# Optimization experiments

Measured on AMD Instinct MI355X. Metric: run time of the kernel, lower is better.

## Reference

```python
import jax, jax.numpy as jnp
import numpy as np

HEADS = 16
DIM_HEAD = 64
SCALE = DIM_HEAD ** -0.5


def setup_inputs() -> dict:
    key = jax.random.key(0)
    k1, k2, k3 = jax.random.split(key, 3)
    B, N, D = 8, 1024, 1024
    x = jax.random.normal(k1, (B, N, D), dtype=jnp.float32)
    # 0/1 keep-mask over the N-1 non-prepended positions
    mask = jax.random.randint(k2, (B, N - 1), 0, 2, dtype=jnp.int32)
    # Linear(dim, 3*inner_dim, bias=False); stored as [dim, 3*inner] so y = x @ W
    w_qkv = jax.random.normal(k3, (D, 3 * HEADS * DIM_HEAD), dtype=jnp.float32) * (D ** -0.5)
    return {"x": x, "mask": mask, "w_qkv": w_qkv}


def reference(x, mask, w_qkv):
    b, n, _ = x.shape
    h, d = HEADS, DIM_HEAD
    qkv = x @ w_qkv                                    # [b, n, 3*h*d]
    q, k, v = jnp.split(qkv, 3, axis=-1)
    to_heads = lambda t: t.reshape(b, n, h, d).transpose(0, 2, 1, 3)  # b h n d
    q, k, v = to_heads(q), to_heads(k), to_heads(v)
    dots = jnp.einsum('bhid,bhjd->bhij', q, k) * SCALE  # [b, h, n, n]
    # F.pad(mask.flatten(1), (1,0), value=1.0) -> prepend a kept position
    m = jnp.pad(mask.reshape(b, -1).astype(jnp.float32), ((0, 0), (1, 0)),
                constant_values=1.0)                    # [b, n]
    dots = dots - 10000.0 * (1.0 - m)[:, None, None, :]
    attn = jax.nn.softmax(dots, axis=-1)
    out = jnp.einsum('bhij,bhjd->bhid', attn, v)        # [b, h, n, d]
    return out.transpose(0, 2, 1, 3).reshape(b, n, h * d)
```

## Files before the change

### kernel.cpp

```cpp
#include <hip/hip_runtime.h>
#include <hip/hip_bf16.h>
#include <stdint.h>

#define HEADS 16
#define DH    64
#define SEQ   1024
#define DIM   1024

typedef __attribute__((ext_vector_type(8))) short bf16x8;
typedef __attribute__((ext_vector_type(4))) float f32x4;
typedef __attribute__((ext_vector_type(16))) float f32x16;
typedef __attribute__((ext_vector_type(4))) unsigned int u32x4;

#define QSCALE_L2 0.18033688011112042f
#define THR_L2 11.541560327111707f
#define PEN_L2 (-14427.0f)

static __device__ __forceinline__ unsigned short f2bf(float f) {
  unsigned u = __builtin_bit_cast(unsigned, f);
  u += 0x7fff + ((u >> 16) & 1);
  return (unsigned short)(u >> 16);
}

static __device__ __forceinline__ float fexp2(float x) {
#if __has_builtin(__builtin_amdgcn_exp2f)
  return __builtin_amdgcn_exp2f(x);
#else
  return exp2f(x);
#endif
}

static __device__ __forceinline__ void gload_lds16(const void* g, void* l) {
  __builtin_amdgcn_global_load_lds(
      (const __attribute__((address_space(1))) unsigned int*)g,
      (__attribute__((address_space(3))) unsigned int*)l,
      16, 0, 0);
}

__global__ __launch_bounds__(256) void build_keep(
    const int* __restrict__ mask, int* __restrict__ inv,
    unsigned short* __restrict__ penc, int* __restrict__ nkeep) {
  const int b = blockIdx.x;
  const int t = threadIdx.x;
  __shared__ int sc[256];
  int kept[4];
  int c = 0;
#pragma unroll
  for (int k = 0; k < 4; ++k) {
    const int j = t * 4 + k;
    const int kp = (j == 0) ? 1 : (mask[b * (SEQ - 1) + j - 1] != 0);
    kept[k] = kp;
    c += kp;
  }
  sc[t] = c;
  __syncthreads();
  for (int off = 1; off < 256; off <<= 1) {
    const int v = (t >= off) ? sc[t - off] : 0;
    __syncthreads();
    sc[t] += v;
    __syncthreads();
  }
  int pos = sc[t] - c;
  const int total = sc[255];
#pragma unroll
  for (int k = 0; k < 4; ++k) {
    const int j = t * 4 + k;
    if (kept[k]) {
      inv[b * SEQ + j] = pos++;
    } else {
      inv[b * SEQ + j] = -1;
    }
  }
#pragma unroll
  for (int k = 0; k < 4; ++k) {
    const int i = t * 4 + k;
    penc[b * SEQ + i] = (i < total) ? (unsigned short)0 : f2bf(PEN_L2);
  }
  if (t == 0) nkeep[b] = total;
}

__global__ __launch_bounds__(256) void cvt_x(
    const float* __restrict__ in, unsigned short* __restrict__ out) {
  const int i = (blockIdx.x * 256 + threadIdx.x) * 4;
  const float4 v = *reinterpret_cast<const float4*>(in + i);
  short4 o;
  o.x = (short)f2bf(v.x);
  o.y = (short)f2bf(v.y);
  o.z = (short)f2bf(v.z);
  o.w = (short)f2bf(v.w);
  *reinterpret_cast<short4*>(out + i) = o;
}

__global__ __launch_bounds__(256) void transpose_w(
    const float* __restrict__ w, unsigned short* __restrict__ wT) {
  __shared__ unsigned short t[64][68];
  const int tid = threadIdx.x;
  const int bk = blockIdx.x;
  const int bn = blockIdx.y;
  const int r = tid >> 4;
  const int c = (tid & 15) * 4;
#pragma unroll
  for (int rr = 0; rr < 64; rr += 16) {
    const float4 v = *reinterpret_cast<const float4*>(
        w + (size_t)(bk * 64 + r + rr) * 3072 + bn * 64 + c);
    t[r + rr][c + 0] = f2bf(v.x);
    t[r + rr][c + 1] = f2bf(v.y);
    t[r + rr][c + 2] = f2bf(v.z);
    t[r + rr][c + 3] = f2bf(v.w);
  }
  __syncthreads();
#pragma unroll
  for (int rr = 0; rr < 64; rr += 16) {
    short4 o;
    o.x = (short)t[c + 0][r + rr];
    o.y = (short)t[c + 1][r + rr];
    o.z = (short)t[c + 2][r + rr];
    o.w = (short)t[c + 3][r + rr];
    *reinterpret_cast<short4*>(
        wT + (size_t)(bn * 64 + r + rr) * 1024 + bk * 64 + c) = o;
  }
}

__global__ __launch_bounds__(256) void qkv_gemm(
    const unsigned short* __restrict__ x, const unsigned short* __restrict__ wT,
    const int* __restrict__ inv,
    unsigned short* __restrict__ Qh, unsigned short* __restrict__ Kc,
    unsigned short* __restrict__ Vtc) {
  __shared__ unsigned short Al[128 * 32];
  __shared__ unsigned short Bl[128 * 32];
  const int tid = threadIdx.x;
  const int lane = tid & 63;
  const int wave = tid >> 6;
  const int m0 = blockIdx.x * 128;
  const int n0 = blockIdx.y * 128;
  const int wm = (wave >> 1) * 64;
  const int wn = (wave & 1) * 64;
  const int l15 = lane & 15;
  const int kb8 = (lane >> 4) * 8;

  f32x4 acc[4][4] = {};

  for (int kt = 0; kt < DIM; kt += 32) {
    __syncthreads();
#pragma unroll
    for (int rnd = 0; rnd < 2; ++rnd) {
      const int off = tid * 16 + rnd * 4096;
      const int row = off >> 6;
      const int kc = (off & 63) >> 1;
      gload_lds16(x + (size_t)(m0 + row) * DIM + kt + kc, (char*)Al + off);
      gload_lds16(wT + (size_t)(n0 + row) * DIM + kt + kc, (char*)Bl + off);
    }
    __syncthreads();
    bf16x8 af[4], bfr[4];
#pragma unroll
    for (int i = 0; i < 4; ++i)
      af[i] = *reinterpret_cast<const bf16x8*>(&Al[(wm + i * 16 + l15) * 32 + kb8]);
#pragma unroll
    for (int j = 0; j < 4; ++j)
      bfr[j] = *reinterpret_cast<const bf16x8*>(&Bl[(wn + j * 16 + l15) * 32 + kb8]);
#pragma unroll
    for (int i = 0; i < 4; ++i)
#pragma unroll
      for (int j = 0; j < 4; ++j)
        acc[i][j] = __builtin_amdgcn_mfma_f32_16x16x32_bf16(af[i], bfr[j], acc[i][j], 0, 0, 0);
  }

  const int sec = n0 >> 10;
  if (sec == 0) {
#pragma unroll
    for (int i = 0; i < 4; ++i) {
#pragma unroll
      for (int j = 0; j < 4; ++j) {
        const int col = n0 + wn + j * 16 + l15;
        const int h = (col >> 6) & 15;
        const int dh = col & 63;
#pragma unroll
        for (int r = 0; r < 4; ++r) {
          const int rowg = m0 + wm + i * 16 + (lane >> 4) * 4 + r;
          const int b = rowg >> 10;
          const int n = rowg & 1023;
          Qh[(((size_t)b * HEADS + h) * SEQ + n) * DH + dh] =
              f2bf(acc[i][j][r] * QSCALE_L2);
        }
      }
    }
  } else {
    int ivr[4][4];
#pragma unroll
    for (int i = 0; i < 4; ++i)
#pragma unroll
      for (int r = 0; r < 4; ++r) {
        const int rowg = m0 + wm + i * 16 + (lane >> 4) * 4 + r;
        ivr[i][r] = inv[(rowg >> 10) * SEQ + (rowg & 1023)];
      }
    if (sec == 1) {
#pragma unroll
      for (int i = 0; i < 4; ++i) {
#pragma unroll
        for (int j = 0; j < 4; ++j) {
          const int col = n0 + wn + j * 16 + l15;
          const int h = (col >> 6) & 15;
          const int dh = col & 63;
#pragma unroll
          for (int r = 0; r < 4; ++r) {
            const int rowg = m0 + wm + i * 16 + (lane >> 4) * 4 + r;
            const int b = rowg >> 10;
            const int iv = ivr[i][r];
            if (iv >= 0)
              Kc[(((size_t)b * HEADS + h) * SEQ + iv) * DH + dh] =
                  f2bf(acc[i][j][r]);
          }
        }
      }
    } else {
#pragma unroll
      for (int i = 0; i < 4; ++i) {
#pragma unroll
        for (int j = 0; j < 4; ++j) {
          const int col = n0 + wn + j * 16 + l15;
          const int h = (col >> 6) & 15;
          const int dh = col & 63;
#pragma unroll
          for (int r = 0; r < 4; ++r) {
            const int rowg = m0 + wm + i * 16 + (lane >> 4) * 4 + r;
            const int b = rowg >> 10;
            const int iv = ivr[i][r];
            if (iv >= 0)
              Vtc[(((size_t)b * HEADS + h) * DH + dh) * SEQ + iv] =
                  f2bf(acc[i][j][r]);
          }
        }
      }
    }
  }
}

__global__ __launch_bounds__(256) void attn_fwd4(
    const unsigned short* __restrict__ Qh, const unsigned short* __restrict__ Kc,
    const unsigned short* __restrict__ Vtc, const unsigned short* __restrict__ penc,
    const int* __restrict__ nkeep, float* __restrict__ out) {
  __shared__ alignas(16) unsigned char Kl[2][8192];
  __shared__ alignas(16) unsigned char Vl[2][8192];
  __shared__ unsigned short penb[SEQ];
  __shared__ float corrw[4][32];
  const int tid = threadIdx.x;
  const int lane = tid & 63;
  const int wave = tid >> 6;
  const int l31 = lane & 31;
  const int hi = lane >> 5;
  const int h8 = hi * 8;
  const bool islo = lane < 32;

  const int bid = ((blockIdx.x & 7) << 7) | (blockIdx.x >> 3);
  const int b = bid >> 7;
  const int hh = (bid >> 3) & 15;
  const int qc = bid & 7;
  const size_t bh = (size_t)b * HEADS + hh;
  const int q0 = qc * 128 + wave * 32;

  const int nk = nkeep[b];
  const int ntile = (nk + 63) >> 6;

  const unsigned short* Q = Qh + bh * SEQ * DH;
  const unsigned short* K = Kc + bh * SEQ * DH;
  const unsigned short* V = Vtc + bh * DH * SEQ;

  auto STAGE = [&](int buf, int kt) {
#pragma unroll
    for (int p = 0; p < 2; ++p) {
      const int off = p * 4096 + tid * 16;
      const int row = off >> 7;
      const int chunk = (off >> 4) & 7;
      const int sch = chunk ^ (row & 7);
      gload_lds16(K + (size_t)(kt + row) * DH + sch * 8, &Kl[buf][off]);
      gload_lds16(V + (size_t)row * SEQ + kt + sch * 8, &Vl[buf][off]);
    }
  };

  STAGE(0, 0);
  for (int j = tid; j < SEQ; j += 256) penb[j] = penc[b * SEQ + j];

  bf16x8 qf[4];
#pragma unroll
  for (int ds = 0; ds < 4; ++ds)
    qf[ds] = *reinterpret_cast<const bf16x8*>(
        Q + (size_t)(q0 + l31) * DH + ds * 16 + h8);

  u32x4 onesu = {0u, 0u, 0u, 0u};
  onesu.x = islo ? 0x3F80u : 0u;
  const bf16x8 onesf = __builtin_bit_cast(bf16x8, onesu);

  f32x16 Od0 = (f32x16)0.f, Od1 = (f32x16)0.f;
  float m_ = 0.f, l_ = 0.f;

  __syncthreads();

  int cur = 0;
  for (int ti = 0; ti < ntile; ++ti) {
    const int kt = ti * 64;
    if (ti + 1 < ntile) STAGE(cur ^ 1, kt + 64);

    f32x16 st0 = (f32x16)0.f, st1 = (f32x16)0.f;
    __builtin_amdgcn_s_setprio(1);
#pragma unroll
    for (int ds = 0; ds < 4; ++ds) {
      const int c0 = (ds * 2 + hi) ^ (l31 & 7);
      const bf16x8 kf0 = *reinterpret_cast<const bf16x8*>(
          &Kl[cur][l31 * 128 + c0 * 16]);
      st0 = __builtin_amdgcn_mfma_f32_32x32x16_bf16(kf0, qf[ds], st0, 0, 0, 0);
      const bf16x8 kf1 = *reinterpret_cast<const bf16x8*>(
          &Kl[cur][(32 + l31) * 128 + c0 * 16]);
      st1 = __builtin_amdgcn_mfma_f32_32x32x16_bf16(kf1, qf[ds], st1, 0, 0, 0);
    }
    __builtin_amdgcn_s_setprio(0);

    {
      const unsigned short pu0 = penb[kt + l31];
      const unsigned short pu1 = penb[kt + 32 + l31];
      u32x4 p0 = {0u, 0u, 0u, 0u}, p1 = {0u, 0u, 0u, 0u};
      p0.x = islo ? (unsigned)pu0 : 0u;
      p1.x = islo ? (unsigned)pu1 : 0u;
      st0 = __builtin_amdgcn_mfma_f32_32x32x16_bf16(
          __builtin_bit_cast(bf16x8, p0), onesf, st0, 0, 0, 0);
      st1 = __builtin_amdgcn_mfma_f32_32x32x16_bf16(
          __builtin_bit_cast(bf16x8, p1), onesf, st1, 0, 0, 0);
    }
    float a[8];
#pragma unroll
    for (int i = 0; i < 8; ++i)
      a[i] = fmaxf(fmaxf(st0[i], st0[i + 8]), fmaxf(st1[i], st1[i + 8]));
#pragma unroll
    for (int k = 4; k >= 1; k >>= 1)
#pragma unroll
      for (int i = 0; i < k; ++i) a[i] = fmaxf(a[i], a[i + k]);
    const float mx = fmaxf(a[0], __shfl_xor(a[0], 32));
    if (!__all(mx <= m_ + THR_L2)) {
      const float mn = fmaxf(m_, mx);
      const float corr = fexp2(m_ - mn);
      m_ = mn;
      l_ *= corr;
      if (islo) corrw[wave][l31] = corr;
      f32x4 cv[4];
#pragma unroll
      for (int j = 0; j < 4; ++j)
        cv[j] = *reinterpret_cast<const f32x4*>(&corrw[wave][j * 8 + (h8 >> 1)]);
#pragma unroll
      for (int r = 0; r < 16; ++r) {
        Od0[r] *= cv[r >> 2][r & 3];
        Od1[r] *= cv[r >> 2][r & 3];
      }
    }
#pragma unroll
    for (int i = 0; i < 16; ++i) {
      st0[i] = fexp2(st0[i] - m_);
      st1[i] = fexp2(st1[i] - m_);
    }
    float s8[8];
#pragma unroll
    for (int i = 0; i < 8; ++i)
      s8[i] = (st0[i] + st0[i + 8]) + (st1[i] + st1[i + 8]);
#pragma unroll
    for (int k = 4; k >= 1; k >>= 1)
#pragma unroll
      for (int i = 0; i < k; ++i) s8[i] += s8[i + k];
    l_ += s8[0] + __shfl_xor(s8[0], 32);
    bf16x8 pf[4];
#pragma unroll
    for (int t = 0; t < 2; ++t) {
#pragma unroll
      for (int bq = 0; bq < 2; ++bq) {
        const int o = 8 * bq;
        float e0 = t ? st1[o + 0] : st0[o + 0], e1 = t ? st1[o + 1] : st0[o + 1];
        float e2 = t ? st1[o + 2] : st0[o + 2], e3 = t ? st1[o + 3] : st0[o + 3];
        float e4 = t ? st1[o + 4] : st0[o + 4], e5 = t ? st1[o + 5] : st0[o + 5];
        float e6 = t ? st1[o + 6] : st0[o + 6], e7 = t ? st1[o + 7] : st0[o + 7];
        unsigned A0, A1, B0, B1;
        asm("v_cvt_pk_bf16_f32 %0, %1, %2" : "=v"(A0) : "v"(e0), "v"(e1));
        asm("v_cvt_pk_bf16_f32 %0, %1, %2" : "=v"(A1) : "v"(e2), "v"(e3));
        asm("v_cvt_pk_bf16_f32 %0, %1, %2" : "=v"(B0) : "v"(e4), "v"(e5));
        asm("v_cvt_pk_bf16_f32 %0, %1, %2" : "=v"(B1) : "v"(e6), "v"(e7));
        asm("v_permlane32_swap_b32 %0, %1\n\ts_nop 1" : "+v"(A0), "+v"(B0));
        asm("v_permlane32_swap_b32 %0, %1\n\ts_nop 1" : "+v"(A1), "+v"(B1));
        u32x4 pk4;
        pk4.x = A0; pk4.y = A1; pk4.z = B0; pk4.w = B1;
        pf[t * 2 + bq] = __builtin_bit_cast(bf16x8, pk4);
      }
    }
    __builtin_amdgcn_s_setprio(1);
#pragma unroll
    for (int kvs = 0; kvs < 4; ++kvs) {
      const int c0 = (kvs * 2 + hi) ^ (l31 & 7);
      const bf16x8 v0 = *reinterpret_cast<const bf16x8*>(
          &Vl[cur][l31 * 128 + c0 * 16]);
      Od0 = __builtin_amdgcn_mfma_f32_32x32x16_bf16(pf[kvs], v0, Od0, 0, 0, 0);
      const bf16x8 v1 = *reinterpret_cast<const bf16x8*>(
          &Vl[cur][(32 + l31) * 128 + c0 * 16]);
      Od1 = __builtin_amdgcn_mfma_f32_32x32x16_bf16(pf[kvs], v1, Od1, 0, 0, 0);
    }
    __builtin_amdgcn_s_setprio(0);

    __syncthreads();
    cur ^= 1;
  }

  if (islo) corrw[wave][l31] = 1.0f / l_;
  f32x4 lv[4];
#pragma unroll
  for (int j = 0; j < 4; ++j)
    lv[j] = *reinterpret_cast<const f32x4*>(&corrw[wave][j * 8 + (h8 >> 1)]);
#pragma unroll
  for (int r = 0; r < 16; ++r) {
    const int q = q0 + (r & 3) + 8 * (r >> 2) + (hi << 2);
    out[((size_t)b * SEQ + q) * (HEADS * DH) + hh * DH + 0 * 32 + l31] =
        Od0[r] * lv[r >> 2][r & 3];
    out[((size_t)b * SEQ + q) * (HEADS * DH) + hh * DH + 1 * 32 + l31] =
        Od1[r] * lv[r >> 2][r & 3];
  }
}

extern "C" void kernel_launch(void* const* d_in, const int* in_sizes, int n_in,
                              void* d_out, int out_size, void* d_ws, size_t ws_size,
                              hipStream_t stream) {
  const float* x = (const float*)d_in[0];
  const int* mask = (const int*)d_in[1];
  const float* w = (const float*)d_in[2];
  float* outp = (float*)d_out;

  char* ws = (char*)d_ws;
  unsigned short* xb   = (unsigned short*)(ws);
  unsigned short* wT   = (unsigned short*)(ws + 16777216);
  unsigned short* Qh   = (unsigned short*)(ws + 23068672);
  unsigned short* Kc   = (unsigned short*)(ws + 39845888);
  unsigned short* Vtc  = (unsigned short*)(ws + 56623104);
  int*            inv  = (int*)(ws + 73400320);
  unsigned short* penc = (unsigned short*)(ws + 73433088);
  int*            nkp  = (int*)(ws + 73449472);

  build_keep<<<dim3(8), 256, 0, stream>>>(mask, inv, penc, nkp);
  cvt_x<<<dim3(8192), 256, 0, stream>>>(x, xb);
  transpose_w<<<dim3(16, 48), 256, 0, stream>>>(w, wT);
  qkv_gemm<<<dim3(64, 24), 256, 0, stream>>>(xb, wT, inv, Qh, Kc, Vtc);
  attn_fwd4<<<dim3(1024), 256, 0, stream>>>(Qh, Kc, Vtc, penc, nkp, outp);
}
```

Baseline: 140.7 us.

## Stage GEMM epilogue through LDS for vector stores, add separate V transpose kernel

The QKV GEMM epilogue now writes each 16x64 accumulator block into shared memory and reads it back as 16-byte rows, so Q, K and V are stored with vectorised, coalesced writes instead of scattered 2-byte stores. The strided transposed V write is replaced by a row-major compacted V buffer plus a new transpose_v kernel that builds the transposed layout in the reused x workspace. The per-key penalty array is removed and the mask penalty is computed inline, applied only on the last key tile. This adds an extra kernel launch and an extra pass over V in exchange for removing uncoalesced global stores.

Result: faster. 131.7 us (-6.4%).

```diff
diff --git a/kernel.cpp b/kernel.cpp
--- a/kernel.cpp
+++ b/kernel.cpp
@@ -38,8 +38,7 @@
 }
 
 __global__ __launch_bounds__(256) void build_keep(
-    const int* __restrict__ mask, int* __restrict__ inv,
-    unsigned short* __restrict__ penc, int* __restrict__ nkeep) {
+    const int* __restrict__ mask, int* __restrict__ inv, int* __restrict__ nkeep) {
   const int b = blockIdx.x;
   const int t = threadIdx.x;
   __shared__ int sc[256];
@@ -65,16 +64,8 @@
 #pragma unroll
   for (int k = 0; k < 4; ++k) {
     const int j = t * 4 + k;
-    if (kept[k]) {
-      inv[b * SEQ + j] = pos++;
-    } else {
-      inv[b * SEQ + j] = -1;
-    }
-  }
-#pragma unroll
-  for (int k = 0; k < 4; ++k) {
-    const int i = t * 4 + k;
-    penc[b * SEQ + i] = (i < total) ? (unsigned short)0 : f2bf(PEN_L2);
+    inv[b * SEQ + j] = kept[k] ? pos : -1;
+    pos += kept[k];
   }
   if (t == 0) nkeep[b] = total;
 }
@@ -125,7 +116,7 @@
     const unsigned short* __restrict__ x, const unsigned short* __restrict__ wT,
     const int* __restrict__ inv,
     unsigned short* __restrict__ Qh, unsigned short* __restrict__ Kc,
-    unsigned short* __restrict__ Vtc) {
+    unsigned short* __restrict__ Vc) {
   __shared__ unsigned short Al[128 * 32];
   __shared__ unsigned short Bl[128 * 32];
   const int tid = threadIdx.x;
@@ -137,6 +128,7 @@
   const int wn = (wave & 1) * 64;
   const int l15 = lane & 15;
   const int kb8 = (lane >> 4) * 8;
+  const int lg4 = (lane >> 4) * 4;
 
   f32x4 acc[4][4] = {};
 
@@ -165,83 +157,75 @@
         acc[i][j] = __builtin_amdgcn_mfma_f32_16x16x32_bf16(af[i], bfr[j], acc[i][j], 0, 0, 0);
   }
 
+  __syncthreads();
+  unsigned short* Sw = (wave < 2 ? Al : Bl) + (wave & 1) * (16 * 72);
   const int sec = n0 >> 10;
-  if (sec == 0) {
-#pragma unroll
-    for (int i = 0; i < 4; ++i) {
-#pragma unroll
-      for (int j = 0; j < 4; ++j) {
-        const int col = n0 + wn + j * 16 + l15;
-        const int h = (col >> 6) & 15;
-        const int dh = col & 63;
-#pragma unroll
-        for (int r = 0; r < 4; ++r) {
-          const int rowg = m0 + wm + i * 16 + (lane >> 4) * 4 + r;
-          const int b = rowg >> 10;
-          const int n = rowg & 1023;
-          Qh[(((size_t)b * HEADS + h) * SEQ + n) * DH + dh] =
-              f2bf(acc[i][j][r] * QSCALE_L2);
+  const float sc = (sec == 0) ? QSCALE_L2 : 1.0f;
+  const int h = ((n0 + wn) >> 6) & 15;
+#pragma unroll
+  for (int i = 0; i < 4; ++i) {
+#pragma unroll
+    for (int j = 0; j < 4; ++j)
+#pragma unroll
+      for (int r = 0; r < 4; ++r)
+        Sw[(lg4 + r) * 72 + j * 16 + l15] = f2bf(acc[i][j][r] * sc);
+#pragma unroll
+    for (int pass = 0; pass < 2; ++pass) {
+      const int row = pass * 8 + (lane >> 3);
+      const int chunk = lane & 7;
+      const bf16x8 vv = *reinterpret_cast<const bf16x8*>(&Sw[row * 72 + chunk * 8]);
+      const int grow = m0 + wm + i * 16 + row;
+      const int b = grow >> 10;
+      const int n = grow & 1023;
+      const size_t bh = (size_t)b * HEADS + h;
+      if (sec == 0) {
+        *reinterpret_cast<bf16x8*>(&Qh[(bh * SEQ + n) * DH + chunk * 8]) = vv;
+      } else {
+        const int iv = inv[b * SEQ + n];
+        if (iv >= 0) {
+          if (sec == 1)
+            *reinterpret_cast<bf16x8*>(&Kc[(bh * SEQ + iv) * DH + chunk * 8]) = vv;
+          else
+            *reinterpret_cast<bf16x8*>(&Vc[(bh * SEQ + iv) * DH + chunk * 8]) = vv;
         }
       }
     }
-  } else {
-    int ivr[4][4];
-#pragma unroll
-    for (int i = 0; i < 4; ++i)
-#pragma unroll
-      for (int r = 0; r < 4; ++r) {
-        const int rowg = m0 + wm + i * 16 + (lane >> 4) * 4 + r;
-        ivr[i][r] = inv[(rowg >> 10) * SEQ + (rowg & 1023)];
-      }
-    if (sec == 1) {
-#pragma unroll
-      for (int i = 0; i < 4; ++i) {
-#pragma unroll
-        for (int j = 0; j < 4; ++j) {
-          const int col = n0 + wn + j * 16 + l15;
-          const int h = (col >> 6) & 15;
-          const int dh = col & 63;
-#pragma unroll
-          for (int r = 0; r < 4; ++r) {
-            const int rowg = m0 + wm + i * 16 + (lane >> 4) * 4 + r;
-            const int b = rowg >> 10;
-            const int iv = ivr[i][r];
-            if (iv >= 0)
-              Kc[(((size_t)b * HEADS + h) * SEQ + iv) * DH + dh] =
-                  f2bf(acc[i][j][r]);
-          }
-        }
-      }
-    } else {
-#pragma unroll
-      for (int i = 0; i < 4; ++i) {
-#pragma unroll
-        for (int j = 0; j < 4; ++j) {
-          const int col = n0 + wn + j * 16 + l15;
-          const int h = (col >> 6) & 15;
-          const int dh = col & 63;
-#pragma unroll
-          for (int r = 0; r < 4; ++r) {
-            const int rowg = m0 + wm + i * 16 + (lane >> 4) * 4 + r;
-            const int b = rowg >> 10;
-            const int iv = ivr[i][r];
-            if (iv >= 0)
-              Vtc[(((size_t)b * HEADS + h) * DH + dh) * SEQ + iv] =
-                  f2bf(acc[i][j][r]);
-          }
-        }
-      }
-    }
-  }
-}
-
-__global__ __launch_bounds__(256) void attn_fwd4(
+  }
+}
+
+__global__ __launch_bounds__(256) void transpose_v(
+    const unsigned short* __restrict__ Vc, unsigned short* __restrict__ Vtc) {
+  __shared__ unsigned short t[64][72];
+  const int tid = threadIdx.x;
+  const int i0 = blockIdx.x * 64;
+  const int bhi = blockIdx.y;
+  const unsigned short* src = Vc + (size_t)bhi * SEQ * DH;
+  unsigned short* dst = Vtc + (size_t)bhi * DH * SEQ;
+  const int r = tid >> 3;
+  const int c = (tid & 7) * 8;
+#pragma unroll
+  for (int rr = 0; rr < 64; rr += 32) {
+    const bf16x8 v = *reinterpret_cast<const bf16x8*>(
+        src + (size_t)(i0 + r + rr) * DH + c);
+    *reinterpret_cast<bf16x8*>(&t[r + rr][c]) = v;
+  }
+  __syncthreads();
+#pragma unroll
+  for (int dd = 0; dd < 64; dd += 32) {
+    const int d = r + dd;
+    bf16x8 o;
+#pragma unroll
+    for (int e = 0; e < 8; ++e) o[e] = (short)t[c + e][d];
+    *reinterpret_cast<bf16x8*>(dst + (size_t)d * SEQ + i0 + c) = o;
+  }
+}
+
+__global__ __launch_bounds__(256) void attn_fwd5(
     const unsigned short* __restrict__ Qh, const unsigned short* __restrict__ Kc,
-    const unsigned short* __restrict__ Vtc, const unsigned short* __restrict__ penc,
+    const unsigned short* __restrict__ Vtc,
     const int* __restrict__ nkeep, float* __restrict__ out) {
   __shared__ alignas(16) unsigned char Kl[2][8192];
   __shared__ alignas(16) unsigned char Vl[2][8192];
-  __shared__ unsigned short penb[SEQ];
   __shared__ float corrw[4][32];
   const int tid = threadIdx.x;
   const int lane = tid & 63;
@@ -278,7 +262,6 @@
   };
 
   STAGE(0, 0);
-  for (int j = tid; j < SEQ; j += 256) penb[j] = penc[b * SEQ + j];
 
   bf16x8 qf[4];
 #pragma unroll
@@ -314,9 +297,10 @@
     }
     __builtin_amdgcn_s_setprio(0);
 
-    {
-      const unsigned short pu0 = penb[kt + l31];
-      const unsigned short pu1 = penb[kt + 32 + l31];
+    if (ti == ntile - 1) {
+      const unsigned short pv = f2bf(PEN_L2);
+      const unsigned short pu0 = (kt + l31 < nk) ? (unsigned short)0 : pv;
+      const unsigned short pu1 = (kt + 32 + l31 < nk) ? (unsigned short)0 : pv;
       u32x4 p0 = {0u, 0u, 0u, 0u}, p1 = {0u, 0u, 0u, 0u};
       p0.x = islo ? (unsigned)pu0 : 0u;
       p1.x = islo ? (unsigned)pu1 : 0u;
@@ -431,14 +415,15 @@
   unsigned short* wT   = (unsigned short*)(ws + 16777216);
   unsigned short* Qh   = (unsigned short*)(ws + 23068672);
   unsigned short* Kc   = (unsigned short*)(ws + 39845888);
-  unsigned short* Vtc  = (unsigned short*)(ws + 56623104);
+  unsigned short* Vc   = (unsigned short*)(ws + 56623104);
   int*            inv  = (int*)(ws + 73400320);
-  unsigned short* penc = (unsigned short*)(ws + 73433088);
-  int*            nkp  = (int*)(ws + 73449472);
-
-  build_keep<<<dim3(8), 256, 0, stream>>>(mask, inv, penc, nkp);
+  int*            nkp  = (int*)(ws + 73433088);
+  unsigned short* Vtc  = xb;
+
+  build_keep<<<dim3(8), 256, 0, stream>>>(mask, inv, nkp);
   cvt_x<<<dim3(8192), 256, 0, stream>>>(x, xb);
   transpose_w<<<dim3(16, 48), 256, 0, stream>>>(w, wT);
-  qkv_gemm<<<dim3(64, 24), 256, 0, stream>>>(xb, wT, inv, Qh, Kc, Vtc);
-  attn_fwd4<<<dim3(1024), 256, 0, stream>>>(Qh, Kc, Vtc, penc, nkp, outp);
-}
+  qkv_gemm<<<dim3(64, 24), 256, 0, stream>>>(xb, wT, inv, Qh, Kc, Vc);
+  transpose_v<<<dim3(16, 128), 256, 0, stream>>>(Vc, Vtc);
+  attn_fwd5<<<dim3(1024), 256, 0, stream>>>(Qh, Kc, Vtc, nkp, outp);
+}
```
